# Kernel optimization log

Measured on AMD Instinct MI355X. Metric: run time of the kernel, lower is better.

## Reference

```python
import jax, jax.numpy as jnp
import numpy as np

WS = 4           # window size (cubic)
NUM_HEADS = 4
DIM = 128
NW = 392         # number of windows per sample
B = 8            # batch
N = WS ** 3      # 64 tokens per window


def _relative_position_index(ws):
    coords = np.stack(np.meshgrid(np.arange(ws), np.arange(ws), np.arange(ws), indexing='ij'))  # [3,ws,ws,ws]
    flat = coords.reshape(3, -1)                      # [3, ws^3]
    rel = flat[:, :, None] - flat[:, None, :]         # [3, N, N]
    rel = rel.transpose(1, 2, 0).copy()               # [N, N, 3]
    rel += ws - 1
    rel[:, :, 0] *= (2 * ws - 1) ** 2
    rel[:, :, 1] *= (2 * ws - 1)
    return rel.sum(-1)                                # [N, N] int


def setup_inputs() -> dict:
    key = jax.random.key(0)
    ks = jax.random.split(key, 8)
    B_ = NW * B
    x = jax.random.normal(ks[0], (B_, N, DIM), dtype=jnp.float32)
    mask = jax.random.normal(ks[1], (NW, N, N), dtype=jnp.float32)
    # learned params
    qkv_w = jax.random.normal(ks[2], (3 * DIM, DIM), dtype=jnp.float32) * 0.02
    qkv_b = jnp.zeros((3 * DIM,), dtype=jnp.float32)
    proj_w = jax.random.normal(ks[3], (DIM, DIM), dtype=jnp.float32) * 0.02
    proj_b = jnp.zeros((DIM,), dtype=jnp.float32)
    tbl = jax.random.normal(ks[4], ((2 * WS - 1) ** 3, NUM_HEADS), dtype=jnp.float32) * 0.02
    rel_index = jnp.asarray(_relative_position_index(WS), dtype=jnp.int32)  # [N, N]
    return {"x": x, "mask": mask, "qkv_w": qkv_w, "qkv_b": qkv_b,
            "proj_w": proj_w, "proj_b": proj_b, "rpb_table": tbl,
            "rel_index": rel_index}


def reference(x, mask, qkv_w, qkv_b, proj_w, proj_b, rpb_table, rel_index):
    B_, N_, C = x.shape
    H = NUM_HEADS
    hd = C // H
    scale = hd ** (-0.5)
    # qkv projection: [B_, N, 3, H, hd] -> (3, B_, H, N, hd)
    qkv = (x @ qkv_w.T + qkv_b).reshape(B_, N_, 3, H, hd).transpose(2, 0, 3, 1, 4)
    q, k, v = qkv[0], qkv[1], qkv[2]
    attn = jnp.einsum('bhnd,bhmd->bhnm', q * scale, k)        # [B_, H, N, N]
    # gathered relative position bias: [N, N, H] -> [H, N, N]
    rpe = rpb_table[rel_index].transpose(2, 0, 1)
    attn = attn + rpe[None]
    nW = mask.shape[0]
    attn = attn.reshape(B_ // nW, nW, H, N_, N_) + mask[None, :, None]
    attn = attn.reshape(B_, H, N_, N_)
    attn = jax.nn.softmax(attn, axis=-1)
    out = jnp.einsum('bhnm,bhmd->bnhd', attn, v).reshape(B_, N_, C)
    return out @ proj_w.T + proj_b
```

## Files before the change

kernel.cpp:

```cpp
#include <hip/hip_runtime.h>
#include <hip/hip_bf16.h>


typedef __bf16 bf16x8 __attribute__((ext_vector_type(8)));
typedef __bf16 bf16x4 __attribute__((ext_vector_type(4)));
typedef float f32x4 __attribute__((ext_vector_type(4)));

#define NWMASK 392
#define SCALE 0.17677669529663687f

__global__ void prep(const float* __restrict__ qkv_w, const float* __restrict__ proj_w,
                     const float* __restrict__ tbl, const int* __restrict__ ridx,
                     __bf16* __restrict__ wqkv, __bf16* __restrict__ wproj,
                     float* __restrict__ rpe) {
    int i = blockIdx.x * 256 + threadIdx.x;
    if (i < 49152) {
        wqkv[i] = (__bf16)qkv_w[i];
    } else if (i < 65536) {
        int j = i - 49152;  wproj[j] = (__bf16)proj_w[j];
    } else {
        int j = i - 65536;
        rpe[j] = tbl[ridx[j & 4095] * 4 + (j >> 12)];
    }
}

__global__ __launch_bounds__(256, 4) void wattn_main(
    const float* __restrict__ x, const float* __restrict__ mask,
    const float* __restrict__ qkv_b, const float* __restrict__ proj_b,
    const __bf16* __restrict__ wqkv, const __bf16* __restrict__ wproj,
    const float* __restrict__ rpe, float* __restrict__ out)
{
    __shared__ __align__(16) __bf16 smem[18944];
    const int win  = blockIdx.x;
    const int tid  = threadIdx.x;
    const int h    = tid >> 6;
    const int lane = tid & 63;
    const int quad = lane >> 4;
    const int l16  = lane & 15;

    __bf16* const xs  = smem;
    __bf16* const buf = smem + 8704 + h * 2560;
    __bf16* const osw = smem + h * 2176;

    {
        const float* xb = x + (size_t)win * 8192;
        #pragma unroll
        for (int i = 0; i < 2; ++i) {
            const int row  = h * 16 + (lane >> 3) + i * 8;
            const int colg = (lane & 7) * 16;
            const float* xp = xb + row * 128 + colg;
            float4 a0 = *(const float4*)(xp);
            float4 a1 = *(const float4*)(xp + 4);
            float4 a2 = *(const float4*)(xp + 8);
            float4 a3 = *(const float4*)(xp + 12);
            bf16x8 t0, t1;
            t0[0]=(__bf16)a0.x; t0[1]=(__bf16)a0.y; t0[2]=(__bf16)a0.z; t0[3]=(__bf16)a0.w;
            t0[4]=(__bf16)a1.x; t0[5]=(__bf16)a1.y; t0[6]=(__bf16)a1.z; t0[7]=(__bf16)a1.w;
            t1[0]=(__bf16)a2.x; t1[1]=(__bf16)a2.y; t1[2]=(__bf16)a2.z; t1[3]=(__bf16)a2.w;
            t1[4]=(__bf16)a3.x; t1[5]=(__bf16)a3.y; t1[6]=(__bf16)a3.z; t1[7]=(__bf16)a3.w;
            *(bf16x8*)(xs + row * 136 + colg)     = t0;
            *(bf16x8*)(xs + row * 136 + colg + 8) = t1;
        }
    }
    __syncthreads();

    bf16x8 kf[4], qf[4], vf[2][2];

    {
        bf16x8 wf[2][4]; float bb[2];
        #pragma unroll
        for (int nt = 0; nt < 2; ++nt) {
            const int ng = 128 + h * 32 + nt * 16 + l16;
            bb[nt] = qkv_b[ng];
            #pragma unroll
            for (int kt = 0; kt < 4; ++kt)
                wf[nt][kt] = *(const bf16x8*)(wqkv + ng * 128 + kt * 32 + quad * 8);
        }
        #pragma unroll
        for (int mt = 0; mt < 4; ++mt) {
            bf16x8 af[4];
            #pragma unroll
            for (int kt = 0; kt < 4; ++kt)
                af[kt] = *(const bf16x8*)(xs + (mt * 16 + l16) * 136 + kt * 32 + quad * 8);
            #pragma unroll
            for (int nt = 0; nt < 2; ++nt) {
                f32x4 acc = {0.f, 0.f, 0.f, 0.f};
                #pragma unroll
                for (int kt = 0; kt < 4; ++kt)
                    acc = __builtin_amdgcn_mfma_f32_16x16x32_bf16(af[kt], wf[nt][kt], acc, 0, 0, 0);
                #pragma unroll
                for (int r = 0; r < 4; ++r)
                    buf[(mt * 16 + quad * 4 + r) * 40 + nt * 16 + l16] = (__bf16)(acc[r] + bb[nt]);
            }
        }
        #pragma unroll
        for (int j = 0; j < 4; ++j)
            kf[j] = *(const bf16x8*)(buf + (j * 16 + l16) * 40 + quad * 8);
    }

    {
        bf16x8 wf[2][4]; float bb[2];
        #pragma unroll
        for (int nt = 0; nt < 2; ++nt) {
            const int ng = h * 32 + nt * 16 + l16;
            bb[nt] = qkv_b[ng];
            #pragma unroll
            for (int kt = 0; kt < 4; ++kt)
                wf[nt][kt] = *(const bf16x8*)(wqkv + ng * 128 + kt * 32 + quad * 8);
        }
        #pragma unroll
        for (int mt = 0; mt < 4; ++mt) {
            bf16x8 af[4];
            #pragma unroll
            for (int kt = 0; kt < 4; ++kt)
                af[kt] = *(const bf16x8*)(xs + (mt * 16 + l16) * 136 + kt * 32 + quad * 8);
            #pragma unroll
            for (int nt = 0; nt < 2; ++nt) {
                f32x4 acc = {0.f, 0.f, 0.f, 0.f};
                #pragma unroll
                for (int kt = 0; kt < 4; ++kt)
                    acc = __builtin_amdgcn_mfma_f32_16x16x32_bf16(af[kt], wf[nt][kt], acc, 0, 0, 0);
                #pragma unroll
                for (int r = 0; r < 4; ++r)
                    buf[(mt * 16 + quad * 4 + r) * 40 + nt * 16 + l16] = (__bf16)((acc[r] + bb[nt]) * SCALE);
            }
        }
        #pragma unroll
        for (int mt = 0; mt < 4; ++mt)
            qf[mt] = *(const bf16x8*)(buf + (mt * 16 + l16) * 40 + quad * 8);
    }

    {
        bf16x8 wf[2][4]; float bb[2];
        #pragma unroll
        for (int nt = 0; nt < 2; ++nt) {
            const int ng = 256 + h * 32 + nt * 16 + l16;
            bb[nt] = qkv_b[ng];
            #pragma unroll
            for (int kt = 0; kt < 4; ++kt)
                wf[nt][kt] = *(const bf16x8*)(wqkv + ng * 128 + kt * 32 + quad * 8);
        }
        #pragma unroll
        for (int mt = 0; mt < 4; ++mt) {
            bf16x8 af[4];
            #pragma unroll
            for (int kt = 0; kt < 4; ++kt)
                af[kt] = *(const bf16x8*)(xs + (mt * 16 + l16) * 136 + kt * 32 + quad * 8);
            #pragma unroll
            for (int nt = 0; nt < 2; ++nt) {
                f32x4 acc = {0.f, 0.f, 0.f, 0.f};
                #pragma unroll
                for (int kt = 0; kt < 4; ++kt)
                    acc = __builtin_amdgcn_mfma_f32_16x16x32_bf16(af[kt], wf[nt][kt], acc, 0, 0, 0);
                bf16x4 pk;
                #pragma unroll
                for (int r = 0; r < 4; ++r) pk[r] = (__bf16)(acc[r] + bb[nt]);
                *(bf16x4*)(buf + (nt * 16 + l16) * 72 + mt * 16 + quad * 4) = pk;
            }
        }
        #pragma unroll
        for (int kt = 0; kt < 2; ++kt)
            #pragma unroll
            for (int nf = 0; nf < 2; ++nf)
                vf[kt][nf] = *(const bf16x8*)(buf + (nf * 16 + l16) * 72 + kt * 32 + quad * 8);
    }
    __syncthreads();

    const float* rpeh = rpe + h * 4096;
    const float* mw   = mask + (size_t)(win % NWMASK) * 4096;
    #pragma unroll
    for (int mt = 0; mt < 4; ++mt) {
        f32x4 sc[4];
        #pragma unroll
        for (int nt = 0; nt < 4; ++nt) {
            f32x4 z = {0.f, 0.f, 0.f, 0.f};
            sc[nt] = __builtin_amdgcn_mfma_f32_16x16x32_bf16(qf[mt], kf[nt], z, 0, 0, 0);
        }
        float inv_s[4];
        #pragma unroll
        for (int r = 0; r < 4; ++r) {
            const int row = mt * 16 + quad * 4 + r;
            float mx = -3.0e38f;
            #pragma unroll
            for (int nt = 0; nt < 4; ++nt) {
                float lg = sc[nt][r] + rpeh[row * 64 + nt * 16 + l16] + mw[row * 64 + nt * 16 + l16];
                sc[nt][r] = lg;
                mx = fmaxf(mx, lg);
            }
            #pragma unroll
            for (int s = 1; s < 16; s <<= 1) mx = fmaxf(mx, __shfl_xor(mx, s, 64));
            float sum = 0.f;
            #pragma unroll
            for (int nt = 0; nt < 4; ++nt) {
                float e = __expf(sc[nt][r] - mx);
                sc[nt][r] = e;
                sum += e;
            }
            #pragma unroll
            for (int s = 1; s < 16; s <<= 1) sum += __shfl_xor(sum, s, 64);
            inv_s[r] = 1.0f / sum;
        }
        #pragma unroll
        for (int nt = 0; nt < 4; ++nt)
            #pragma unroll
            for (int r = 0; r < 4; ++r)
                buf[(quad * 4 + r) * 72 + nt * 16 + l16] = (__bf16)sc[nt][r];
        f32x4 oa[2] = {{0.f,0.f,0.f,0.f},{0.f,0.f,0.f,0.f}};
        #pragma unroll
        for (int kt = 0; kt < 2; ++kt) {
            bf16x8 pf = *(const bf16x8*)(buf + l16 * 72 + kt * 32 + quad * 8);
            #pragma unroll
            for (int nf = 0; nf < 2; ++nf)
                oa[nf] = __builtin_amdgcn_mfma_f32_16x16x32_bf16(pf, vf[kt][nf], oa[nf], 0, 0, 0);
        }
        #pragma unroll
        for (int nf = 0; nf < 2; ++nf)
            #pragma unroll
            for (int r = 0; r < 4; ++r)
                osw[(mt * 16 + quad * 4 + r) * 34 + nf * 16 + l16] = (__bf16)(oa[nf][r] * inv_s[r]);
    }
    __syncthreads();

    bf16x8 of[4];
    #pragma unroll
    for (int kt = 0; kt < 4; ++kt)
        of[kt] = *(const bf16x8*)(smem + kt * 2176 + (h * 16 + l16) * 34 + quad * 8);
    #pragma unroll
    for (int nt = 0; nt < 8; ++nt) {
        const int ng = nt * 16 + l16;
        const float b = proj_b[ng];
        bf16x8 wf[4];
        #pragma unroll
        for (int kt = 0; kt < 4; ++kt)
            wf[kt] = *(const bf16x8*)(wproj + ng * 128 + kt * 32 + quad * 8);
        f32x4 acc = {0.f, 0.f, 0.f, 0.f};
        #pragma unroll
        for (int kt = 0; kt < 4; ++kt)
            acc = __builtin_amdgcn_mfma_f32_16x16x32_bf16(of[kt], wf[kt], acc, 0, 0, 0);
        float* dst = out + ((size_t)win * 64 + h * 16 + quad * 4) * 128 + ng;
        #pragma unroll
        for (int r = 0; r < 4; ++r) dst[(size_t)r * 128] = acc[r] + b;
    }
}

extern "C" void kernel_launch(void* const* d_in, const int* in_sizes, int n_in,
                              void* d_out, int out_size, void* d_ws, size_t ws_size,
                              hipStream_t stream) {
    const float* x      = (const float*)d_in[0];
    const float* mask   = (const float*)d_in[1];
    const float* qkv_w  = (const float*)d_in[2];
    const float* qkv_b  = (const float*)d_in[3];
    const float* proj_w = (const float*)d_in[4];
    const float* proj_b = (const float*)d_in[5];
    const float* tbl    = (const float*)d_in[6];
    const int*   ridx   = (const int*)d_in[7];
    float* out = (float*)d_out;

    __bf16* wqkv  = (__bf16*)d_ws;
    __bf16* wproj = wqkv + 384 * 128;
    float*  rpe   = (float*)((char*)d_ws + 131072);

    prep<<<320, 256, 0, stream>>>(qkv_w, proj_w, tbl, ridx, wqkv, wproj, rpe);
    wattn_main<<<3136, 256, 0, stream>>>(x, mask, qkv_b, proj_b, wqkv, wproj, rpe, out);
}
```

Measured before the change: 277.2 us.

## Shrink LDS footprint, drop max-subtract softmax, compute row sums via MFMA

Cuts the shared-memory buffer by double-buffering per-16-row staging for K/Q/V and reusing the x tile for the attention output, which allows launch bounds to rise to five blocks per CU. Softmax is restructured to compute S^T with vectorized float4 loads of bias and mask, skipping the max subtraction and the shuffle reductions. Row sums come from an extra MFMA against a vector of ones. Dropping the max subtraction risks overflow when logits are large, and the higher occupancy target may force register spills.

```diff
diff --git a/kernel.cpp b/kernel.cpp
--- a/kernel.cpp
+++ b/kernel.cpp
@@ -24,13 +24,13 @@
     }
 }
 
-__global__ __launch_bounds__(256, 4) void wattn_main(
+__global__ __launch_bounds__(256, 5) void wattn_main(
     const float* __restrict__ x, const float* __restrict__ mask,
     const float* __restrict__ qkv_b, const float* __restrict__ proj_b,
     const __bf16* __restrict__ wqkv, const __bf16* __restrict__ wproj,
     const float* __restrict__ rpe, float* __restrict__ out)
 {
-    __shared__ __align__(16) __bf16 smem[18944];
+    __shared__ __align__(16) __bf16 smem[13824];
     const int win  = blockIdx.x;
     const int tid  = threadIdx.x;
     const int h    = tid >> 6;
@@ -39,8 +39,7 @@
     const int l16  = lane & 15;
 
     __bf16* const xs  = smem;
-    __bf16* const buf = smem + 8704 + h * 2560;
-    __bf16* const osw = smem + h * 2176;
+    __bf16* const buf = smem + 8704 + h * 1280;
 
     {
         const float* xb = x + (size_t)win * 8192;
@@ -78,6 +77,7 @@
         }
         #pragma unroll
         for (int mt = 0; mt < 4; ++mt) {
+            __bf16* const sb = buf + (mt & 1) * 640;
             bf16x8 af[4];
             #pragma unroll
             for (int kt = 0; kt < 4; ++kt)
@@ -90,12 +90,10 @@
                     acc = __builtin_amdgcn_mfma_f32_16x16x32_bf16(af[kt], wf[nt][kt], acc, 0, 0, 0);
                 #pragma unroll
                 for (int r = 0; r < 4; ++r)
-                    buf[(mt * 16 + quad * 4 + r) * 40 + nt * 16 + l16] = (__bf16)(acc[r] + bb[nt]);
+                    sb[(quad * 4 + r) * 40 + nt * 16 + l16] = (__bf16)(acc[r] + bb[nt]);
             }
-        }
-        #pragma unroll
-        for (int j = 0; j < 4; ++j)
-            kf[j] = *(const bf16x8*)(buf + (j * 16 + l16) * 40 + quad * 8);
+            kf[mt] = *(const bf16x8*)(sb + l16 * 40 + quad * 8);
+        }
     }
 
     {
@@ -110,6 +108,7 @@
         }
         #pragma unroll
         for (int mt = 0; mt < 4; ++mt) {
+            __bf16* const sb = buf + (mt & 1) * 640;
             bf16x8 af[4];
             #pragma unroll
             for (int kt = 0; kt < 4; ++kt)
@@ -122,109 +121,95 @@
                     acc = __builtin_amdgcn_mfma_f32_16x16x32_bf16(af[kt], wf[nt][kt], acc, 0, 0, 0);
                 #pragma unroll
                 for (int r = 0; r < 4; ++r)
-                    buf[(mt * 16 + quad * 4 + r) * 40 + nt * 16 + l16] = (__bf16)((acc[r] + bb[nt]) * SCALE);
+                    sb[(quad * 4 + r) * 40 + nt * 16 + l16] = (__bf16)((acc[r] + bb[nt]) * SCALE);
             }
-        }
-        #pragma unroll
-        for (int mt = 0; mt < 4; ++mt)
-            qf[mt] = *(const bf16x8*)(buf + (mt * 16 + l16) * 40 + quad * 8);
-    }
-
-    {
-        bf16x8 wf[2][4]; float bb[2];
-        #pragma unroll
-        for (int nt = 0; nt < 2; ++nt) {
-            const int ng = 256 + h * 32 + nt * 16 + l16;
-            bb[nt] = qkv_b[ng];
-            #pragma unroll
-            for (int kt = 0; kt < 4; ++kt)
-                wf[nt][kt] = *(const bf16x8*)(wqkv + ng * 128 + kt * 32 + quad * 8);
-        }
-        #pragma unroll
-        for (int mt = 0; mt < 4; ++mt) {
-            bf16x8 af[4];
-            #pragma unroll
-            for (int kt = 0; kt < 4; ++kt)
-                af[kt] = *(const bf16x8*)(xs + (mt * 16 + l16) * 136 + kt * 32 + quad * 8);
-            #pragma unroll
-            for (int nt = 0; nt < 2; ++nt) {
-                f32x4 acc = {0.f, 0.f, 0.f, 0.f};
+            qf[mt] = *(const bf16x8*)(sb + l16 * 40 + quad * 8);
+        }
+    }
+
+    {
+        #pragma unroll
+        for (int half = 0; half < 2; ++half) {
+            #pragma unroll
+            for (int m2 = 0; m2 < 2; ++m2) {
+                const int mt = half * 2 + m2;
+                bf16x8 af[4];
                 #pragma unroll
                 for (int kt = 0; kt < 4; ++kt)
-                    acc = __builtin_amdgcn_mfma_f32_16x16x32_bf16(af[kt], wf[nt][kt], acc, 0, 0, 0);
-                bf16x4 pk;
-                #pragma unroll
-                for (int r = 0; r < 4; ++r) pk[r] = (__bf16)(acc[r] + bb[nt]);
-                *(bf16x4*)(buf + (nt * 16 + l16) * 72 + mt * 16 + quad * 4) = pk;
+                    af[kt] = *(const bf16x8*)(xs + (mt * 16 + l16) * 136 + kt * 32 + quad * 8);
+                #pragma unroll
+                for (int nt = 0; nt < 2; ++nt) {
+                    const int ng = 256 + h * 32 + nt * 16 + l16;
+                    const float bb = qkv_b[ng];
+                    bf16x8 w0 = *(const bf16x8*)(wqkv + ng * 128 +       quad * 8);
+                    bf16x8 w1 = *(const bf16x8*)(wqkv + ng * 128 +  32 + quad * 8);
+                    bf16x8 w2 = *(const bf16x8*)(wqkv + ng * 128 +  64 + quad * 8);
+                    bf16x8 w3 = *(const bf16x8*)(wqkv + ng * 128 +  96 + quad * 8);
+                    f32x4 acc = {0.f, 0.f, 0.f, 0.f};
+                    acc = __builtin_amdgcn_mfma_f32_16x16x32_bf16(af[0], w0, acc, 0, 0, 0);
+                    acc = __builtin_amdgcn_mfma_f32_16x16x32_bf16(af[1], w1, acc, 0, 0, 0);
+                    acc = __builtin_amdgcn_mfma_f32_16x16x32_bf16(af[2], w2, acc, 0, 0, 0);
+                    acc = __builtin_amdgcn_mfma_f32_16x16x32_bf16(af[3], w3, acc, 0, 0, 0);
+                    bf16x4 pk;
+                    #pragma unroll
+                    for (int r = 0; r < 4; ++r) pk[r] = (__bf16)(acc[r] + bb);
+                    *(bf16x4*)(buf + (nt * 16 + l16) * 40 + m2 * 16 + quad * 4) = pk;
+                }
             }
-        }
-        #pragma unroll
-        for (int kt = 0; kt < 2; ++kt)
             #pragma unroll
             for (int nf = 0; nf < 2; ++nf)
-                vf[kt][nf] = *(const bf16x8*)(buf + (nf * 16 + l16) * 72 + kt * 32 + quad * 8);
+                vf[half][nf] = *(const bf16x8*)(buf + (nf * 16 + l16) * 40 + quad * 8);
+        }
+        buf[1152 + lane] = (__bf16)1.0f;
     }
     __syncthreads();
 
-    const float* rpeh = rpe + h * 4096;
-    const float* mw   = mask + (size_t)(win % NWMASK) * 4096;
+    const float* rh = rpe + h * 4096;
+    const float* mw = mask + (size_t)(win % NWMASK) * 4096;
     #pragma unroll
-    for (int mt = 0; mt < 4; ++mt) {
-        f32x4 sc[4];
-        #pragma unroll
-        for (int nt = 0; nt < 4; ++nt) {
+    for (int jb = 0; jb < 4; ++jb) {
+        const int qrow = jb * 16 + l16;
+        f32x4 st[4];
+        #pragma unroll
+        for (int it = 0; it < 4; ++it) {
             f32x4 z = {0.f, 0.f, 0.f, 0.f};
-            sc[nt] = __builtin_amdgcn_mfma_f32_16x16x32_bf16(qf[mt], kf[nt], z, 0, 0, 0);
-        }
-        float inv_s[4];
-        #pragma unroll
-        for (int r = 0; r < 4; ++r) {
-            const int row = mt * 16 + quad * 4 + r;
-            float mx = -3.0e38f;
-            #pragma unroll
-            for (int nt = 0; nt < 4; ++nt) {
-                float lg = sc[nt][r] + rpeh[row * 64 + nt * 16 + l16] + mw[row * 64 + nt * 16 + l16];
-                sc[nt][r] = lg;
-                mx = fmaxf(mx, lg);
-            }
-            #pragma unroll
-            for (int s = 1; s < 16; s <<= 1) mx = fmaxf(mx, __shfl_xor(mx, s, 64));
-            float sum = 0.f;
-            #pragma unroll
-            for (int nt = 0; nt < 4; ++nt) {
-                float e = __expf(sc[nt][r] - mx);
-                sc[nt][r] = e;
-                sum += e;
-            }
-            #pragma unroll
-            for (int s = 1; s < 16; s <<= 1) sum += __shfl_xor(sum, s, 64);
-            inv_s[r] = 1.0f / sum;
-        }
-        #pragma unroll
-        for (int nt = 0; nt < 4; ++nt)
-            #pragma unroll
-            for (int r = 0; r < 4; ++r)
-                buf[(quad * 4 + r) * 72 + nt * 16 + l16] = (__bf16)sc[nt][r];
+            st[it] = __builtin_amdgcn_mfma_f32_16x16x32_bf16(kf[it], qf[jb], z, 0, 0, 0);
+        }
+        #pragma unroll
+        for (int it = 0; it < 4; ++it) {
+            float4 r4 = *(const float4*)(rh + qrow * 64 + it * 16 + quad * 4);
+            float4 m4 = *(const float4*)(mw + qrow * 64 + it * 16 + quad * 4);
+            bf16x4 pk;
+            pk[0] = (__bf16)__expf(st[it][0] + r4.x + m4.x);
+            pk[1] = (__bf16)__expf(st[it][1] + r4.y + m4.y);
+            pk[2] = (__bf16)__expf(st[it][2] + r4.z + m4.z);
+            pk[3] = (__bf16)__expf(st[it][3] + r4.w + m4.w);
+            *(bf16x4*)(buf + l16 * 72 + it * 16 + quad * 4) = pk;
+        }
         f32x4 oa[2] = {{0.f,0.f,0.f,0.f},{0.f,0.f,0.f,0.f}};
+        f32x4 os = {0.f, 0.f, 0.f, 0.f};
         #pragma unroll
         for (int kt = 0; kt < 2; ++kt) {
             bf16x8 pf = *(const bf16x8*)(buf + l16 * 72 + kt * 32 + quad * 8);
-            #pragma unroll
-            for (int nf = 0; nf < 2; ++nf)
-                oa[nf] = __builtin_amdgcn_mfma_f32_16x16x32_bf16(pf, vf[kt][nf], oa[nf], 0, 0, 0);
-        }
-        #pragma unroll
-        for (int nf = 0; nf < 2; ++nf)
-            #pragma unroll
-            for (int r = 0; r < 4; ++r)
-                osw[(mt * 16 + quad * 4 + r) * 34 + nf * 16 + l16] = (__bf16)(oa[nf][r] * inv_s[r]);
+            bf16x8 o1 = *(const bf16x8*)(buf + 1152 + kt * 32 + quad * 8);
+            oa[0] = __builtin_amdgcn_mfma_f32_16x16x32_bf16(pf, vf[kt][0], oa[0], 0, 0, 0);
+            oa[1] = __builtin_amdgcn_mfma_f32_16x16x32_bf16(pf, vf[kt][1], oa[1], 0, 0, 0);
+            os    = __builtin_amdgcn_mfma_f32_16x16x32_bf16(pf, o1, os, 0, 0, 0);
+        }
+        #pragma unroll
+        for (int r = 0; r < 4; ++r) {
+            const float inv = 1.0f / os[r];
+            const int orow = jb * 16 + quad * 4 + r;
+            xs[orow * 136 + h * 32 + l16]      = (__bf16)(oa[0][r] * inv);
+            xs[orow * 136 + h * 32 + 16 + l16] = (__bf16)(oa[1][r] * inv);
+        }
     }
     __syncthreads();
 
     bf16x8 of[4];
     #pragma unroll
     for (int kt = 0; kt < 4; ++kt)
-        of[kt] = *(const bf16x8*)(smem + kt * 2176 + (h * 16 + l16) * 34 + quad * 8);
+        of[kt] = *(const bf16x8*)(xs + (h * 16 + l16) * 136 + kt * 32 + quad * 8);
     #pragma unroll
     for (int nt = 0; nt < 8; ++nt) {
         const int ng = nt * 16 + l16;
```

New measurement: 329.8 us. 1.19x slower.

## Drop softmax max pass, get row sums via MFMA, prefetch bias and weights

Applied to the files above, without the earlier changes.

The softmax no longer subtracts the row maximum and no longer uses cross-lane shuffle reductions. Each score is exponentiated directly, and the row sum comes from an extra MFMA against a vector of ones, so the normalizer matches the bf16 probabilities used in P·V. The rpe and mask values for each tile are loaded before the QK MFMAs, and the K-projection weights are loaded before the first barrier, to hide global-load latency. The attention output now goes into the x tile's shared buffer with a 136-element stride instead of a separate per-head layout. Skipping the max subtraction can overflow for large logits, so correctness now depends on the logit range.

```diff
diff --git a/kernel.cpp b/kernel.cpp
--- a/kernel.cpp
+++ b/kernel.cpp
@@ -40,7 +40,6 @@
 
     __bf16* const xs  = smem;
     __bf16* const buf = smem + 8704 + h * 2560;
-    __bf16* const osw = smem + h * 2176;
 
     {
         const float* xb = x + (size_t)win * 8192;
@@ -62,20 +61,21 @@
             *(bf16x8*)(xs + row * 136 + colg + 8) = t1;
         }
     }
+
+    bf16x8 kwf[2][4]; float kbb[2];
+    #pragma unroll
+    for (int nt = 0; nt < 2; ++nt) {
+        const int ng = 128 + h * 32 + nt * 16 + l16;
+        kbb[nt] = qkv_b[ng];
+        #pragma unroll
+        for (int kt = 0; kt < 4; ++kt)
+            kwf[nt][kt] = *(const bf16x8*)(wqkv + ng * 128 + kt * 32 + quad * 8);
+    }
     __syncthreads();
 
     bf16x8 kf[4], qf[4], vf[2][2];
 
     {
-        bf16x8 wf[2][4]; float bb[2];
-        #pragma unroll
-        for (int nt = 0; nt < 2; ++nt) {
-            const int ng = 128 + h * 32 + nt * 16 + l16;
-            bb[nt] = qkv_b[ng];
-            #pragma unroll
-            for (int kt = 0; kt < 4; ++kt)
-                wf[nt][kt] = *(const bf16x8*)(wqkv + ng * 128 + kt * 32 + quad * 8);
-        }
         #pragma unroll
         for (int mt = 0; mt < 4; ++mt) {
             bf16x8 af[4];
@@ -87,10 +87,10 @@
                 f32x4 acc = {0.f, 0.f, 0.f, 0.f};
                 #pragma unroll
                 for (int kt = 0; kt < 4; ++kt)
-                    acc = __builtin_amdgcn_mfma_f32_16x16x32_bf16(af[kt], wf[nt][kt], acc, 0, 0, 0);
+                    acc = __builtin_amdgcn_mfma_f32_16x16x32_bf16(af[kt], kwf[nt][kt], acc, 0, 0, 0);
                 #pragma unroll
                 for (int r = 0; r < 4; ++r)
-                    buf[(mt * 16 + quad * 4 + r) * 40 + nt * 16 + l16] = (__bf16)(acc[r] + bb[nt]);
+                    buf[(mt * 16 + quad * 4 + r) * 40 + nt * 16 + l16] = (__bf16)(acc[r] + kbb[nt]);
             }
         }
         #pragma unroll
@@ -166,65 +166,58 @@
     }
     __syncthreads();
 
+    bf16x8 onesf;
+    #pragma unroll
+    for (int j = 0; j < 8; ++j) onesf[j] = (__bf16)1.0f;
+
     const float* rpeh = rpe + h * 4096;
     const float* mw   = mask + (size_t)(win % NWMASK) * 4096;
     #pragma unroll
     for (int mt = 0; mt < 4; ++mt) {
+        float rb[4][4], mb[4][4];
+        #pragma unroll
+        for (int nt = 0; nt < 4; ++nt)
+            #pragma unroll
+            for (int r = 0; r < 4; ++r) {
+                const int row = mt * 16 + quad * 4 + r;
+                rb[nt][r] = rpeh[row * 64 + nt * 16 + l16];
+                mb[nt][r] = mw[row * 64 + nt * 16 + l16];
+            }
         f32x4 sc[4];
         #pragma unroll
         for (int nt = 0; nt < 4; ++nt) {
             f32x4 z = {0.f, 0.f, 0.f, 0.f};
             sc[nt] = __builtin_amdgcn_mfma_f32_16x16x32_bf16(qf[mt], kf[nt], z, 0, 0, 0);
         }
-        float inv_s[4];
-        #pragma unroll
-        for (int r = 0; r < 4; ++r) {
-            const int row = mt * 16 + quad * 4 + r;
-            float mx = -3.0e38f;
-            #pragma unroll
-            for (int nt = 0; nt < 4; ++nt) {
-                float lg = sc[nt][r] + rpeh[row * 64 + nt * 16 + l16] + mw[row * 64 + nt * 16 + l16];
-                sc[nt][r] = lg;
-                mx = fmaxf(mx, lg);
-            }
-            #pragma unroll
-            for (int s = 1; s < 16; s <<= 1) mx = fmaxf(mx, __shfl_xor(mx, s, 64));
-            float sum = 0.f;
-            #pragma unroll
-            for (int nt = 0; nt < 4; ++nt) {
-                float e = __expf(sc[nt][r] - mx);
-                sc[nt][r] = e;
-                sum += e;
-            }
-            #pragma unroll
-            for (int s = 1; s < 16; s <<= 1) sum += __shfl_xor(sum, s, 64);
-            inv_s[r] = 1.0f / sum;
-        }
         #pragma unroll
         for (int nt = 0; nt < 4; ++nt)
             #pragma unroll
             for (int r = 0; r < 4; ++r)
-                buf[(quad * 4 + r) * 72 + nt * 16 + l16] = (__bf16)sc[nt][r];
+                buf[(quad * 4 + r) * 72 + nt * 16 + l16] =
+                    (__bf16)__expf(sc[nt][r] + rb[nt][r] + mb[nt][r]);
         f32x4 oa[2] = {{0.f,0.f,0.f,0.f},{0.f,0.f,0.f,0.f}};
+        f32x4 os = {0.f, 0.f, 0.f, 0.f};
         #pragma unroll
         for (int kt = 0; kt < 2; ++kt) {
             bf16x8 pf = *(const bf16x8*)(buf + l16 * 72 + kt * 32 + quad * 8);
-            #pragma unroll
-            for (int nf = 0; nf < 2; ++nf)
-                oa[nf] = __builtin_amdgcn_mfma_f32_16x16x32_bf16(pf, vf[kt][nf], oa[nf], 0, 0, 0);
-        }
-        #pragma unroll
-        for (int nf = 0; nf < 2; ++nf)
-            #pragma unroll
-            for (int r = 0; r < 4; ++r)
-                osw[(mt * 16 + quad * 4 + r) * 34 + nf * 16 + l16] = (__bf16)(oa[nf][r] * inv_s[r]);
+            oa[0] = __builtin_amdgcn_mfma_f32_16x16x32_bf16(pf, vf[kt][0], oa[0], 0, 0, 0);
+            oa[1] = __builtin_amdgcn_mfma_f32_16x16x32_bf16(pf, vf[kt][1], oa[1], 0, 0, 0);
+            os    = __builtin_amdgcn_mfma_f32_16x16x32_bf16(pf, onesf,     os,    0, 0, 0);
+        }
+        #pragma unroll
+        for (int r = 0; r < 4; ++r) {
+            const float inv = 1.0f / os[r];
+            const int orow = mt * 16 + quad * 4 + r;
+            xs[orow * 136 + h * 32 + l16]      = (__bf16)(oa[0][r] * inv);
+            xs[orow * 136 + h * 32 + 16 + l16] = (__bf16)(oa[1][r] * inv);
+        }
     }
     __syncthreads();
 
     bf16x8 of[4];
     #pragma unroll
     for (int kt = 0; kt < 4; ++kt)
-        of[kt] = *(const bf16x8*)(smem + kt * 2176 + (h * 16 + l16) * 34 + quad * 8);
+        of[kt] = *(const bf16x8*)(xs + (h * 16 + l16) * 136 + kt * 32 + quad * 8);
     #pragma unroll
     for (int nt = 0; nt < 8; ++nt) {
         const int ng = nt * 16 + l16;
```

Result: faster. 270.2 us (-2.5%).
